# Optimization experiments

Measured on AMD Instinct MI355X. Metric: run time of the kernel, lower is better.

## Reference

```python
import jax, jax.numpy as jnp
import numpy as np

K = 64                 # count_bins
HID = 32               # hidden width of conditioner MLP
PARAM_DIM = 4 * K - 1  # widths(K) + heights(K) + derivs(K-1) + lambdas(K)
BOUND = 3.0
MIN_BIN_W = 1e-3
MIN_BIN_H = 1e-3
MIN_DERIV = 1e-3
N = 1_048_576


def setup_inputs() -> dict:
    key = jax.random.key(0)
    ks = jax.random.split(key, 5)

    def init_lin(k, fan_in, fan_out):
        bnd = 1.0 / np.sqrt(fan_in)
        kw, kb = jax.random.split(k)
        W = jax.random.uniform(kw, (fan_in, fan_out), jnp.float32, -bnd, bnd)
        b = jax.random.uniform(kb, (fan_out,), jnp.float32, -bnd, bnd)
        return W, b

    W1, b1 = init_lin(ks[0], 1, HID)
    W2, b2 = init_lin(ks[1], HID, HID)
    W3, b3 = init_lin(ks[2], HID, PARAM_DIM)
    x = jax.random.normal(ks[3], (N,), jnp.float32)
    condx = jax.random.normal(ks[4], (N,), jnp.float32)
    return {"x": x, "condx": condx, "W1": W1, "b1": b1,
            "W2": W2, "b2": b2, "W3": W3, "b3": b3}


def _normalize_bins(un, min_frac, n):
    # softmax widths -> cumulative knots on [-BOUND, BOUND]
    w = min_frac + (1.0 - min_frac * K) * jax.nn.softmax(un, axis=-1)
    cum = jnp.concatenate([jnp.zeros((n, 1), un.dtype), jnp.cumsum(w, -1)], -1)
    cum = 2.0 * BOUND * cum - BOUND
    cum = cum.at[:, 0].set(-BOUND).at[:, -1].set(BOUND)
    return cum, cum[:, 1:] - cum[:, :-1]


def _spline(x, params):
    # monotonic linear-rational spline (pyro order='linear'), elementwise on x
    n = x.shape[0]
    w_un = params[:, :K]
    h_un = params[:, K:2 * K]
    d_un = params[:, 2 * K:3 * K - 1]
    l_un = params[:, 3 * K - 1:]

    cumw, bw = _normalize_bins(w_un, MIN_BIN_W, n)   # knots/widths in x
    cumh, bh = _normalize_bins(h_un, MIN_BIN_H, n)   # knots/heights in y

    one = jnp.ones((n, 1), x.dtype)
    derivs = jnp.concatenate(
        [one, MIN_DERIV + jax.nn.softplus(d_un), one], -1)  # [n, K+1]
    lambdas = 0.95 * jax.nn.sigmoid(l_un) + 0.025            # [n, K]

    inside = (x >= -BOUND) & (x <= BOUND)
    xc = jnp.clip(x, -BOUND, BOUND)
    # bin search: index of bin containing xc
    idx = jnp.clip(jnp.sum(xc[:, None] >= cumw, axis=-1) - 1, 0, K - 1)[:, None]

    g = lambda a, i: jnp.take_along_axis(a, i, axis=-1)[:, 0]
    xk, wk = g(cumw, idx), g(bw, idx)
    yk, hk = g(cumh, idx), g(bh, idx)
    d0, d1 = g(derivs, idx), g(derivs, idx + 1)
    lam = g(lambdas, idx)

    slope = hk / wk
    wb = jnp.sqrt(d0 / d1)                                   # wa == 1
    wc = (lam * d0 + (1.0 - lam) * wb * d1) / slope
    ya, yb = yk, yk + hk
    yc = ((1.0 - lam) * ya + lam * wb * yb) / ((1.0 - lam) + lam * wb)

    theta = (xc - xk) / wk
    left = theta <= lam
    num = jnp.where(left, ya * (lam - theta) + wc * yc * theta,
                    wc * yc * (1.0 - theta) + wb * yb * (theta - lam))
    den = jnp.where(left, (lam - theta) + wc * theta,
                    wc * (1.0 - theta) + wb * (theta - lam))
    y_in = num / den
    dnum = jnp.where(left, wc * lam * (yc - ya),
                     wb * wc * (1.0 - lam) * (yb - yc))
    ld_in = jnp.log(dnum) - 2.0 * jnp.log(jnp.abs(den)) - jnp.log(wk)

    y = jnp.where(inside, y_in, x)       # identity outside support
    ld = jnp.where(inside, ld_in, 0.0)
    return y, ld


def reference(x, condx, W1, b1, W2, b2, W3, b3):
    # conditioner MLP: cond scalar -> 4K-1 unnormalized spline params
    h = jax.nn.relu(condx[:, None] @ W1 + b1)
    h = jax.nn.relu(h @ W2 + b2)
    params = h @ W3 + b3                 # [N, 4K-1]
    y, logdet = _spline(x, params)
    return y, logdet
```

## Files before the change

kernel.cpp:

```cpp
#include <hip/hip_runtime.h>
#include <math.h>

#define BOUND 3.0f
#define LOG2E 1.4426950408889634f
#define LN2 0.6931471805599453f
#define CINV 0.17806267806267807f

typedef _Float16 half8 __attribute__((ext_vector_type(8)));
typedef _Float16 half4 __attribute__((ext_vector_type(4)));
typedef _Float16 half2v __attribute__((ext_vector_type(2)));
typedef float f32x4 __attribute__((ext_vector_type(4)));
typedef float f32x2 __attribute__((ext_vector_type(2)));

__device__ __forceinline__ float fexp2(float x) { return __builtin_amdgcn_exp2f(x); }
__device__ __forceinline__ float flog2(float x) { return __builtin_amdgcn_logf(x); }
__device__ __forceinline__ float frcp(float x)  { return __builtin_amdgcn_rcpf(x); }

__device__ __forceinline__ float hsum2(half2v a, float c) {
    const half2v ones = {(_Float16)1.f, (_Float16)1.f};
    return __builtin_amdgcn_fdot2(a, ones, c, false);
}

__device__ __forceinline__ half2v pkcvt(float a, float b) {
    return __builtin_bit_cast(half2v, __builtin_amdgcn_cvt_pkrtz(a, b));
}

__global__ void prep_kernel(const float* __restrict__ W2, const float* __restrict__ W3,
                            const float* __restrict__ b3,
                            _Float16* __restrict__ aW2, _Float16* __restrict__ aW3,
                            float* __restrict__ b3s) {
    int tid = blockIdx.x * blockDim.x + threadIdx.x;
    int nth = gridDim.x * blockDim.x;
    for (int i = tid; i < 16 * 64 * 8; i += nth) {
        int t = i & 7, l = (i >> 3) & 63, m = i >> 9;
        int k = 8 * (l >> 4) + t, col = 16 * m + (l & 15);
        float v = (col < 255) ? W3[k * 255 + col] : 0.f;
        if (m < 8) v *= LOG2E;
        aW3[i] = (_Float16)v;
    }
    for (int i = tid; i < 2 * 64 * 8; i += nth) {
        int t = i & 7, l = (i >> 3) & 63, m = i >> 9;
        int k = 8 * (l >> 4) + t, col = 16 * m + (l & 15);
        aW2[i] = (_Float16)W2[k * 32 + col];
    }
    for (int i = tid; i < 255; i += nth)
        b3s[i] = b3[i] * ((i < 128) ? LOG2E : 1.f);
}

__global__ __launch_bounds__(64, 4) void spline_kernel(
    const float* __restrict__ x_in, const float* __restrict__ cond_in,
    const float* __restrict__ W1, const float* __restrict__ b1,
    const float* __restrict__ b2, const float* __restrict__ b3s,
    const _Float16* __restrict__ aW2, const _Float16* __restrict__ aW3,
    float* __restrict__ out, int N) {

    __shared__ float sbuf[64 * 32];

    const int l = threadIdx.x;
    const int j = l & 15, g = l >> 4;
    const int sx = l & 7;
    const int ksw = j & 7;
    const int gown = blockIdx.x * 64 + l;
    const int ic = (gown < N) ? gown : (N - 1);

    float* buf = sbuf;
    _Float16* bufh = (_Float16*)sbuf;

    float cx = cond_in[ic];
    float x = x_in[ic];

    f32x2 w1p[4], b1p[4];
#pragma unroll
    for (int p = 0; p < 4; p++) {
        w1p[p] = *(const f32x2*)(W1 + 8 * g + 2 * p);
        b1p[p] = *(const f32x2*)(b1 + 8 * g + 2 * p);
    }

    half8 h1hi[4], h1lo[4];
#pragma unroll
    for (int n = 0; n < 4; n++) {
        float c = __shfl(cx, 16 * n + j, 64);
        f32x2 c2 = {c, c};
        const f32x2 z2 = {0.f, 0.f};
#pragma unroll
        for (int p = 0; p < 4; p++) {
            f32x2 h = c2 * w1p[p] + b1p[p];
            h = __builtin_elementwise_max(h, z2);
            half2v hi = pkcvt(h.x, h.y);
            f32x2 hf = {(float)hi[0], (float)hi[1]};
            f32x2 lo = h - hf;
            half2v lov = pkcvt(lo.x, lo.y);
            h1hi[n][2 * p] = hi[0];  h1hi[n][2 * p + 1] = hi[1];
            h1lo[n][2 * p] = lov[0]; h1lo[n][2 * p + 1] = lov[1];
        }
    }

    half8 a2[2];
    a2[0] = *(const half8*)(aW2 + (0 * 64 + l) * 8);
    a2[1] = *(const half8*)(aW2 + (1 * 64 + l) * 8);

#pragma unroll
    for (int m = 0; m < 2; m++) {
        float4 bb = *(const float4*)(b2 + 16 * m + 4 * g);
        f32x4 binit = {bb.x, bb.y, bb.z, bb.w};
#pragma unroll
        for (int n = 0; n < 4; n++) {
            f32x4 acc = binit;
            acc = __builtin_amdgcn_mfma_f32_16x16x32_f16(a2[m], h1lo[n], acc, 0, 0, 0);
            acc = __builtin_amdgcn_mfma_f32_16x16x32_f16(a2[m], h1hi[n], acc, 0, 0, 0);
            const f32x2 z2 = {0.f, 0.f};
            f32x2 v01 = {acc[0], acc[1]}, v23 = {acc[2], acc[3]};
            v01 = __builtin_elementwise_max(v01, z2);
            v23 = __builtin_elementwise_max(v23, z2);
            half2v h01 = pkcvt(v01.x, v01.y);
            half2v h23 = pkcvt(v23.x, v23.y);
            f32x2 f01 = {(float)h01[0], (float)h01[1]};
            f32x2 f23 = {(float)h23[0], (float)h23[1]};
            f32x2 l01 = v01 - f01, l23 = v23 - f23;
            half2v q01 = pkcvt(l01.x, l01.y);
            half2v q23 = pkcvt(l23.x, l23.y);
            half4 hv = {h01[0], h01[1], h23[0], h23[1]};
            half4 lv = {q01[0], q01[1], q23[0], q23[1]};
            int rb = (16 * n + j) * 64;
            *(half4*)(bufh + rb + (((2 * m + (g >> 1)) ^ ksw) << 3) + ((g & 1) << 2)) = hv;
            *(half4*)(bufh + rb + (((4 + 2 * m + (g >> 1)) ^ ksw) << 3) + ((g & 1) << 2)) = lv;
        }
    }

    half8 bhi[4], blo[4];
#pragma unroll
    for (int n = 0; n < 4; n++) {
        int rb = (16 * n + j) * 64;
        bhi[n] = *(const half8*)(bufh + rb + ((g ^ ksw) << 3));
        blo[n] = *(const half8*)(bufh + rb + (((4 + g) ^ ksw) << 3));
    }

    bool inside = (x >= -BOUND) && (x <= BOUND);
    float xc = fminf(fmaxf(x, -BOUND), BOUND);

    f32x4 wv[16];
#pragma unroll
    for (int s = 0; s < 2; s++) {
#pragma unroll
        for (int mm = 0; mm < 2; mm++) {
            int m = 2 * s + mm;
            half8 a = *(const half8*)(aW3 + (m * 64 + l) * 8);
            float4 bb = *(const float4*)(b3s + 16 * m + 4 * g);
            f32x4 binit = {bb.x, bb.y, bb.z, bb.w};
#pragma unroll
            for (int n = 0; n < 4; n++) {
                f32x4 acc = binit;
                acc = __builtin_amdgcn_mfma_f32_16x16x32_f16(a, blo[n], acc, 0, 0, 0);
                acc = __builtin_amdgcn_mfma_f32_16x16x32_f16(a, bhi[n], acc, 0, 0, 0);
                f32x4 e = {fexp2(acc[0]), fexp2(acc[1]), fexp2(acc[2]), fexp2(acc[3])};
                *(f32x4*)(buf + (16 * n + j) * 32 + (((4 * mm + g) ^ ksw) << 2)) = e;
            }
        }
#pragma unroll
        for (int t = 0; t < 8; t++)
            wv[8 * s + t] = *(const f32x4*)(buf + l * 32 + ((t ^ sx) << 2));
    }

    int idx; float idxf, xk, wk;
    {
        float G[16];
        float run = 0.f;
#pragma unroll
        for (int t = 0; t < 16; t++) {
            run += (wv[t][0] + wv[t][1]) + (wv[t][2] + wv[t][3]);
            G[t] = run;
        }
        float tot = G[15];
        float rcptot = frcp(tot);
        float rr = (xc + BOUND) * tot * CINV;
        float dr1 = 0.0010683761f * tot;
        float dr4 = 4.f * dr1;
        float r = rr, Gsel = 0.f;
        int qidx = 0;
#pragma unroll
        for (int t = 0; t < 15; t++) {
            r -= dr4;
            bool c = (G[t] <= r);
            qidx += c ? 1 : 0;
            Gsel = c ? G[t] : Gsel;
        }
        f32x4 fv = wv[0];
#pragma unroll
        for (int t = 1; t < 16; t++) fv = (qidx == t) ? wv[t] : fv;
        float e0 = fv[0], e1 = fv[1], e2 = fv[2], e3 = fv[3];
        float qf = (float)qidx;
        float rq = fmaf(-qf, dr4, rr);
        float p1 = Gsel + e0, p2 = p1 + e1, p3 = p2 + e2;
        bool c1 = (p1 <= rq - dr1);
        bool c2 = (p2 <= fmaf(-2.f, dr1, rq));
        bool c3 = (p3 <= fmaf(-3.f, dr1, rq));
        idx = 4 * qidx + (c1 ? 1 : 0) + (c2 ? 1 : 0) + (c3 ? 1 : 0);
        float Pk = c1 ? p1 : Gsel; Pk = c2 ? p2 : Pk; Pk = c3 ? p3 : Pk;
        float ek = c1 ? e1 : e0;   ek = c2 ? e2 : ek; ek = c3 ? e3 : ek;
        idxf = (float)idx;
        xk = fmaf(0.006f, idxf, -BOUND) + 5.616f * Pk * rcptot;
        wk = fmaf(5.616f * rcptot, ek, 0.006f);
        wk = (idx == 63) ? (BOUND - xk) : wk;
    }

#pragma unroll
    for (int m = 0; m < 4; m++) {
        half8 a = *(const half8*)(aW3 + ((m + 4) * 64 + l) * 8);
        float4 bb = *(const float4*)(b3s + 64 + 16 * m + 4 * g);
        f32x4 binit = {bb.x, bb.y, bb.z, bb.w};
#pragma unroll
        for (int n = 0; n < 4; n++) {
            f32x4 acc = binit;
            acc = __builtin_amdgcn_mfma_f32_16x16x32_f16(a, bhi[n], acc, 0, 0, 0);
            half2v e01 = pkcvt(fexp2(acc[0]), fexp2(acc[1]));
            half2v e23 = pkcvt(fexp2(acc[2]), fexp2(acc[3]));
            half4 e = {e01[0], e01[1], e23[0], e23[1]};
            *(half4*)(bufh + (16 * n + j) * 64 +
                      (((2 * m + (g >> 1)) ^ ksw) << 3) + ((g & 1) << 2)) = e;
        }
    }

    float yk, hk;
    {
        int qh = idx >> 2, rh = idx & 3;
        float toth = 0.f, Gq = 0.f;
#pragma unroll
        for (int t = 0; t < 8; t++) {
            half8 hv = *(const half8*)(bufh + l * 64 + ((t ^ sx) << 3));
            half2v* hp = (half2v*)&hv;
            float gs0 = hsum2(hp[0], hsum2(hp[1], 0.f));
            float gs1 = hsum2(hp[2], hsum2(hp[3], 0.f));
            toth += gs0 + gs1;
            Gq += (2 * t < qh) ? gs0 : 0.f;
            Gq += (2 * t + 1 < qh) ? gs1 : 0.f;
        }
        half4 fv = *(const half4*)(bufh + l * 64 + (((qh >> 1) ^ sx) << 3) + ((qh & 1) << 2));
        float f0 = (float)fv[0], f1 = (float)fv[1], f2 = (float)fv[2], f3 = (float)fv[3];
        float Sh = Gq;
        Sh += (rh >= 1) ? f0 : 0.f;
        Sh += (rh >= 2) ? f1 : 0.f;
        Sh += (rh >= 3) ? f2 : 0.f;
        float x01 = (rh & 1) ? f1 : f0;
        float x23 = (rh & 1) ? f3 : f2;
        float eidx = (rh & 2) ? x23 : x01;
        float chh = 5.616f * frcp(toth);
        yk = fmaf(0.006f, idxf, -BOUND) + chh * Sh;
        hk = fmaf(chh, eidx, 0.006f);
        hk = (idx == 63) ? (BOUND - yk) : hk;
    }

    const int c0 = (idx > 0) ? (idx - 1) : 0;
    const int rc0a = (c0 < 32) ? c0 : 31;
    const int rc0b = (c0 >= 32) ? (c0 - 32) : 0;
    const int rc1a = (idx < 32) ? idx : 31;
    const int rc1b = (idx >= 32) ? (idx - 32) : 0;
    float v0a, v0b, v1a, v1b, vl191, vla, vlb;
#pragma unroll
    for (int s = 0; s < 4; s++) {
#pragma unroll
        for (int mm = 0; mm < 2; mm++) {
            half8 a = *(const half8*)(aW3 + ((8 + 2 * s + mm) * 64 + l) * 8);
#pragma unroll
            for (int n = 0; n < 4; n++) {
                f32x4 acc = {0.f, 0.f, 0.f, 0.f};
                acc = __builtin_amdgcn_mfma_f32_16x16x32_f16(a, bhi[n], acc, 0, 0, 0);
                *(f32x4*)(buf + (16 * n + j) * 32 + (((4 * mm + g) ^ ksw) << 2)) = acc;
            }
        }
        if (s == 0) {
            v0a = buf[l * 32 + (((rc0a >> 2) ^ sx) << 2) + (rc0a & 3)];
            v1a = buf[l * 32 + (((rc1a >> 2) ^ sx) << 2) + (rc1a & 3)];
        } else if (s == 1) {
            v0b = buf[l * 32 + (((rc0b >> 2) ^ sx) << 2) + (rc0b & 3)];
            v1b = buf[l * 32 + (((rc1b >> 2) ^ sx) << 2) + (rc1b & 3)];
            vl191 = buf[l * 32 + ((7 ^ sx) << 2) + 3];
        } else if (s == 2) {
            vla = buf[l * 32 + (((rc0a >> 2) ^ sx) << 2) + (rc0a & 3)];
        } else {
            vlb = buf[l * 32 + (((rc0b >> 2) ^ sx) << 2) + (rc0b & 3)];
        }
    }
    float accd0 = ((c0 < 32) ? v0a : v0b) + b3s[127 + idx];
    float accd1 = ((idx < 32) ? v1a : v1b) + b3s[(idx < 63) ? (128 + idx) : 191];
    float lsel = (c0 < 32) ? vla : vlb;
    float accl = ((idx == 0) ? vl191 : lsel) + b3s[191 + idx];

    float e0t = fexp2(-fabsf(accd0) * LOG2E);
    float sp0 = fmaxf(accd0, 0.f) + LN2 * flog2(1.f + e0t);
    float e1t = fexp2(-fabsf(accd1) * LOG2E);
    float sp1 = fmaxf(accd1, 0.f) + LN2 * flog2(1.f + e1t);
    float d0 = (idx == 0)  ? 1.f : (0.001f + sp0);
    float d1 = (idx == 63) ? 1.f : (0.001f + sp1);
    float sig = frcp(1.f + fexp2(-accl * LOG2E));
    float lam = fmaf(0.95f, sig, 0.025f);

    float rwk = frcp(wk);
    float wb = sqrtf(d0 * frcp(d1));
    float wc = fmaf(lam, d0, (1.f - lam) * wb * d1) * wk * frcp(hk);
    float ya = yk, yb = yk + hk;
    float yc = fmaf(1.f - lam, ya, lam * wb * yb) * frcp(fmaf(lam, wb, 1.f - lam));
    float theta = (xc - xk) * rwk;
    bool left = theta <= lam;
    float num = left ? fmaf(ya, lam - theta, wc * yc * theta)
                     : fmaf(wc * yc, 1.f - theta, wb * yb * (theta - lam));
    float den = left ? fmaf(wc, theta, lam - theta)
                     : fmaf(wc, 1.f - theta, wb * (theta - lam));
    float y_in = num * frcp(den);
    float dnum = left ? (wc * lam * (yc - ya))
                      : (wb * wc * (1.f - lam) * (yb - yc));
    float ld_in = LN2 * (flog2(dnum) - 2.f * flog2(fabsf(den)) - flog2(wk));

    if (gown < N) {
        out[gown]     = inside ? y_in : x;
        out[N + gown] = inside ? ld_in : 0.f;
    }
}

extern "C" void kernel_launch(void* const* d_in, const int* in_sizes, int n_in,
                              void* d_out, int out_size, void* d_ws, size_t ws_size,
                              hipStream_t stream) {
    const float* x  = (const float*)d_in[0];
    const float* cx = (const float*)d_in[1];
    const float* W1 = (const float*)d_in[2];
    const float* b1 = (const float*)d_in[3];
    const float* W2 = (const float*)d_in[4];
    const float* b2 = (const float*)d_in[5];
    const float* W3 = (const float*)d_in[6];
    const float* b3 = (const float*)d_in[7];
    int N = in_sizes[0];

    _Float16* aW3 = (_Float16*)d_ws;
    _Float16* aW2 = aW3 + 16 * 64 * 8;
    float* b3s = (float*)(aW2 + 2 * 64 * 8);
    float* out = (float*)d_out;

    hipLaunchKernelGGL(prep_kernel, dim3(8), dim3(256), 0, stream, W2, W3, b3, aW2, aW3, b3s);
    hipLaunchKernelGGL(spline_kernel, dim3((N + 63) / 64), dim3(64), 0, stream,
                       x, cx, W1, b1, b2, b3s, aW2, aW3, out, N);
}
```

Measured before the change: 59.56 us.

## Compute derivative and lambda params via per-thread gathered dot products instead of MFMA

Instead of running 32 MFMAs to compute all 128 derivative/lambda logits per row and then picking three values out of LDS, each thread gathers the three needed W3 columns (pre-transposed to fp16 in the prep kernel) and computes just those three logits with fdot2 against its own hidden vector read from LDS. This removes most of the matrix work and LDS round trips in the last stage. In exchange it adds divergent per-thread global loads of 12 half8 weight vectors and 48 serial fdot2 operations per thread, plus extra register pressure.

```diff
diff --git a/kernel.cpp b/kernel.cpp
--- a/kernel.cpp
+++ b/kernel.cpp
@@ -20,6 +20,9 @@
     const half2v ones = {(_Float16)1.f, (_Float16)1.f};
     return __builtin_amdgcn_fdot2(a, ones, c, false);
 }
+__device__ __forceinline__ float fdot2(half2v a, half2v b, float c) {
+    return __builtin_amdgcn_fdot2(a, b, c, false);
+}
 
 __device__ __forceinline__ half2v pkcvt(float a, float b) {
     return __builtin_bit_cast(half2v, __builtin_amdgcn_cvt_pkrtz(a, b));
@@ -28,7 +31,7 @@
 __global__ void prep_kernel(const float* __restrict__ W2, const float* __restrict__ W3,
                             const float* __restrict__ b3,
                             _Float16* __restrict__ aW2, _Float16* __restrict__ aW3,
-                            float* __restrict__ b3s) {
+                            float* __restrict__ b3s, _Float16* __restrict__ gw) {
     int tid = blockIdx.x * blockDim.x + threadIdx.x;
     int nth = gridDim.x * blockDim.x;
     for (int i = tid; i < 16 * 64 * 8; i += nth) {
@@ -45,6 +48,10 @@
     }
     for (int i = tid; i < 255; i += nth)
         b3s[i] = b3[i] * ((i < 128) ? LOG2E : 1.f);
+    for (int i = tid; i < 128 * 32; i += nth) {
+        int c = i >> 5, k = i & 31;
+        gw[i] = (_Float16)W3[k * 255 + 127 + c];
+    }
 }
 
 __global__ __launch_bounds__(64, 4) void spline_kernel(
@@ -52,6 +59,7 @@
     const float* __restrict__ W1, const float* __restrict__ b1,
     const float* __restrict__ b2, const float* __restrict__ b3s,
     const _Float16* __restrict__ aW2, const _Float16* __restrict__ aW3,
+    const _Float16* __restrict__ gw,
     float* __restrict__ out, int N) {
 
     __shared__ float sbuf[64 * 32];
@@ -134,6 +142,10 @@
         bhi[n] = *(const half8*)(bufh + rb + ((g ^ ksw) << 3));
         blo[n] = *(const half8*)(bufh + rb + (((4 + g) ^ ksw) << 3));
     }
+    half8 myh2[4];
+#pragma unroll
+    for (int t = 0; t < 4; t++)
+        myh2[t] = *(const half8*)(bufh + l * 64 + ((t ^ sx) << 3));
 
     bool inside = (x >= -BOUND) && (x <= BOUND);
     float xc = fminf(fmaxf(x, -BOUND), BOUND);
@@ -203,6 +215,22 @@
         wk = (idx == 63) ? (BOUND - xk) : wk;
     }
 
+    const int cD0 = idx;
+    const int cD1 = (idx < 63) ? (idx + 1) : 64;
+    const int cL  = 64 + idx;
+    half8 wD0a = *(const half8*)(gw + cD0 * 32);
+    half8 wD0b = *(const half8*)(gw + cD0 * 32 + 8);
+    half8 wD0c = *(const half8*)(gw + cD0 * 32 + 16);
+    half8 wD0d = *(const half8*)(gw + cD0 * 32 + 24);
+    half8 wD1a = *(const half8*)(gw + cD1 * 32);
+    half8 wD1b = *(const half8*)(gw + cD1 * 32 + 8);
+    half8 wD1c = *(const half8*)(gw + cD1 * 32 + 16);
+    half8 wD1d = *(const half8*)(gw + cD1 * 32 + 24);
+    half8 wLa  = *(const half8*)(gw + cL * 32);
+    half8 wLb  = *(const half8*)(gw + cL * 32 + 8);
+    half8 wLc  = *(const half8*)(gw + cL * 32 + 16);
+    half8 wLd  = *(const half8*)(gw + cL * 32 + 24);
+
 #pragma unroll
     for (int m = 0; m < 4; m++) {
         half8 a = *(const half8*)(aW3 + ((m + 4) * 64 + l) * 8);
@@ -249,41 +277,36 @@
         hk = (idx == 63) ? (BOUND - yk) : hk;
     }
 
-    const int c0 = (idx > 0) ? (idx - 1) : 0;
-    const int rc0a = (c0 < 32) ? c0 : 31;
-    const int rc0b = (c0 >= 32) ? (c0 - 32) : 0;
-    const int rc1a = (idx < 32) ? idx : 31;
-    const int rc1b = (idx >= 32) ? (idx - 32) : 0;
-    float v0a, v0b, v1a, v1b, vl191, vla, vlb;
-#pragma unroll
-    for (int s = 0; s < 4; s++) {
-#pragma unroll
-        for (int mm = 0; mm < 2; mm++) {
-            half8 a = *(const half8*)(aW3 + ((8 + 2 * s + mm) * 64 + l) * 8);
-#pragma unroll
-            for (int n = 0; n < 4; n++) {
-                f32x4 acc = {0.f, 0.f, 0.f, 0.f};
-                acc = __builtin_amdgcn_mfma_f32_16x16x32_f16(a, bhi[n], acc, 0, 0, 0);
-                *(f32x4*)(buf + (16 * n + j) * 32 + (((4 * mm + g) ^ ksw) << 2)) = acc;
-            }
-        }
-        if (s == 0) {
-            v0a = buf[l * 32 + (((rc0a >> 2) ^ sx) << 2) + (rc0a & 3)];
-            v1a = buf[l * 32 + (((rc1a >> 2) ^ sx) << 2) + (rc1a & 3)];
-        } else if (s == 1) {
-            v0b = buf[l * 32 + (((rc0b >> 2) ^ sx) << 2) + (rc0b & 3)];
-            v1b = buf[l * 32 + (((rc1b >> 2) ^ sx) << 2) + (rc1b & 3)];
-            vl191 = buf[l * 32 + ((7 ^ sx) << 2) + 3];
-        } else if (s == 2) {
-            vla = buf[l * 32 + (((rc0a >> 2) ^ sx) << 2) + (rc0a & 3)];
-        } else {
-            vlb = buf[l * 32 + (((rc0b >> 2) ^ sx) << 2) + (rc0b & 3)];
-        }
-    }
-    float accd0 = ((c0 < 32) ? v0a : v0b) + b3s[127 + idx];
-    float accd1 = ((idx < 32) ? v1a : v1b) + b3s[(idx < 63) ? (128 + idx) : 191];
-    float lsel = (c0 < 32) ? vla : vlb;
-    float accl = ((idx == 0) ? vl191 : lsel) + b3s[191 + idx];
+    float accd0 = b3s[127 + idx];
+    float accd1 = b3s[(idx < 63) ? (128 + idx) : 191];
+    float accl  = b3s[191 + idx];
+    {
+        half2v* h0 = (half2v*)&myh2[0];
+        half2v* h1 = (half2v*)&myh2[1];
+        half2v* h2p = (half2v*)&myh2[2];
+        half2v* h3 = (half2v*)&myh2[3];
+        half2v* d0a = (half2v*)&wD0a; half2v* d0b = (half2v*)&wD0b;
+        half2v* d0c = (half2v*)&wD0c; half2v* d0d = (half2v*)&wD0d;
+        half2v* d1a = (half2v*)&wD1a; half2v* d1b = (half2v*)&wD1b;
+        half2v* d1c = (half2v*)&wD1c; half2v* d1d = (half2v*)&wD1d;
+        half2v* la = (half2v*)&wLa; half2v* lb = (half2v*)&wLb;
+        half2v* lc = (half2v*)&wLc; half2v* ld = (half2v*)&wLd;
+#pragma unroll
+        for (int p = 0; p < 4; p++) {
+            accd0 = fdot2(h0[p], d0a[p], accd0);
+            accd0 = fdot2(h1[p], d0b[p], accd0);
+            accd0 = fdot2(h2p[p], d0c[p], accd0);
+            accd0 = fdot2(h3[p], d0d[p], accd0);
+            accd1 = fdot2(h0[p], d1a[p], accd1);
+            accd1 = fdot2(h1[p], d1b[p], accd1);
+            accd1 = fdot2(h2p[p], d1c[p], accd1);
+            accd1 = fdot2(h3[p], d1d[p], accd1);
+            accl  = fdot2(h0[p], la[p], accl);
+            accl  = fdot2(h1[p], lb[p], accl);
+            accl  = fdot2(h2p[p], lc[p], accl);
+            accl  = fdot2(h3[p], ld[p], accl);
+        }
+    }
 
     float e0t = fexp2(-fabsf(accd0) * LOG2E);
     float sp0 = fmaxf(accd0, 0.f) + LN2 * flog2(1.f + e0t);
@@ -332,9 +355,10 @@
     _Float16* aW3 = (_Float16*)d_ws;
     _Float16* aW2 = aW3 + 16 * 64 * 8;
     float* b3s = (float*)(aW2 + 2 * 64 * 8);
+    _Float16* gw = (_Float16*)(b3s + 256);
     float* out = (float*)d_out;
 
-    hipLaunchKernelGGL(prep_kernel, dim3(8), dim3(256), 0, stream, W2, W3, b3, aW2, aW3, b3s);
+    hipLaunchKernelGGL(prep_kernel, dim3(8), dim3(256), 0, stream, W2, W3, b3, aW2, aW3, b3s, gw);
     hipLaunchKernelGGL(spline_kernel, dim3((N + 63) / 64), dim3(64), 0, stream,
-                       x, cx, W1, b1, b2, b3s, aW2, aW3, out, N);
-}
+                       x, cx, W1, b1, b2, b3s, aW2, aW3, gw, out, N);
+}
```

After: 62.26 us. 4.5% more time.
